# Kernel tuning notes

Hardware: AMD Instinct MI355X
Metric: run time of the kernel (lower is better)

The kernel has to match this reference:

```python
import jax, jax.numpy as jnp
import numpy as np

DT = 0.02
TMAX = 3.0
NUM_T = 151  # arange(0, Tmax+dt, dt) -> indices 0..150, 150*dt == Tmax == nonspike
THRESH = 1.0
TIMELINE = jnp.arange(NUM_T, dtype=jnp.float32) * DT          # [T]
TIMELINE_REV = jnp.flip(TIMELINE) + 0.1                        # [T]


def linear_spike_fwd(ti, W):
    """ti: [B, Fin] spike times; W: [Fout, Fin] -> out: [B, Fout] spike times."""
    # ramp: relu(t - ti)  -> [B, Fin, T]
    tmp = jax.nn.relu(TIMELINE[None, None, :] - ti[:, :, None])
    # membrane voltage: mem[b,j,t] = sum_i W[j,i] * tmp[b,i,t]  -> [B, Fout, T]
    mem = jnp.einsum('bit,ji->bjt', tmp, W)
    binary = (mem >= THRESH).astype(jnp.float32)
    binary = binary.at[:, :, -1].set(1.0)  # force spike at last timestep
    # reversed-timeline weighting makes argmax pick the FIRST spike index
    idx = jnp.argmax(binary * TIMELINE_REV, axis=2)
    return idx.astype(jnp.float32) * DT


def setup_inputs() -> dict:
    key = jax.random.key(0)
    k1, k2, k3 = jax.random.split(key, 3)
    B, F0, F1, F2 = 64, 1876, 1024, 10
    ti = jax.random.uniform(k1, (B, F0), dtype=jnp.float32)  # spike times in [0,1)
    W1 = 0.002 + 0.002 * jax.random.normal(k2, (F1, F0), dtype=jnp.float32)
    W2 = 0.001 + 0.001 * jax.random.normal(k3, (F2, F1), dtype=jnp.float32)
    return {"ti": ti, "W1": W1, "W2": W2}


def reference(ti, W1, W2):
    h1 = linear_spike_fwd(ti, W1)
    h2 = linear_spike_fwd(h1, W2)
    return h2
```

## Files before the change

### kernel.cpp

```cpp
#include <hip/hip_runtime.h>
#include <stdint.h>

namespace {

constexpr int   B_    = 64;
constexpr int   F0_   = 1876;
constexpr int   F1_   = 1024;
constexpr int   F2_   = 10;
constexpr int   NT_   = 151;
constexpr float DT_   = 0.02f;
constexpr int   NSTR_ = 2048;
constexpr int   CHUNK_= 256;
constexpr int   NGRP_ = 32;
constexpr int   NB1_  = 51;
constexpr float SCL_  = 67108864.0f;
constexpr float ISCL_ = 1.0f / 67108864.0f;

constexpr size_t OFF_W1T  = 0;
constexpr size_t OFF_PAIR = 7688192;
constexpr size_t OFF_IDX1 = OFF_PAIR + 1048576;

__global__ __launch_bounds__(256) void k_w1t(const float* __restrict__ W1,
                                             float* __restrict__ W1T) {
  __shared__ float tile[64][65];
  const int i0 = blockIdx.x * 64;
  const int j0 = blockIdx.y * 64;
  const int t  = threadIdx.x;
  const int c  = t & 63, r4 = t >> 6;
  for (int jj = r4; jj < 64; jj += 4) {
    int i = i0 + c;
    float v = (i < F0_) ? W1[(size_t)(j0 + jj) * F0_ + i] : 0.0f;
    tile[c][jj] = v;
  }
  __syncthreads();
  for (int ii = r4; ii < 64; ii += 4) {
    int i = i0 + ii;
    if (i <= F0_) W1T[(size_t)i * F1_ + j0 + c] = tile[ii][c];
  }
}

__global__ __launch_bounds__(256) void k_sort1(const float* __restrict__ ti,
                                               uint2* __restrict__ sPair) {
  __shared__ uint32_t hist[256][NB1_];
  __shared__ uint32_t bstart[NB1_ + 1];
  const int b = blockIdx.x, t = threadIdx.x;
  for (int k = 0; k < NB1_; ++k) hist[t][k] = 0;
  __syncthreads();

  const float* tib = ti + (size_t)b * F0_;
  const int n0 = t * 8;
  const int n1 = (n0 + 8 < F0_) ? n0 + 8 : F0_;
  for (int n = n0; n < n1; ++n) {
    int k = (int)ceilf(tib[n] * 50.0f);
    k = k < 0 ? 0 : (k > 50 ? 50 : k);
    hist[t][k]++;
  }
  __syncthreads();

  if (t < NB1_) {
    uint32_t run = 0;
    for (int c = 0; c < 256; ++c) { uint32_t x = hist[c][t]; hist[c][t] = run; run += x; }
    bstart[t + 1] = run;
  }
  __syncthreads();
  if (t == 0) {
    bstart[0] = 0;
    uint32_t acc = 0;
    for (int k = 0; k < NB1_; ++k) { uint32_t c = bstart[k + 1]; bstart[k + 1] = acc + c; acc += c; }
  }
  __syncthreads();

  uint2* out = sPair + (size_t)b * NSTR_;
  for (int n = n0; n < n1; ++n) {
    float v = tib[n];
    int k = (int)ceilf(v * 50.0f);
    k = k < 0 ? 0 : (k > 50 ? 50 : k);
    uint32_t pos = bstart[k] + hist[t][k]++;
    out[pos] = make_uint2(((uint32_t)n << 12) | (uint32_t)k, __float_as_uint(v));
  }
  for (int s = t; s < NSTR_ - F0_; s += 256)
    out[F0_ + s] = make_uint2(((uint32_t)F0_ << 12) | 80u, __float_as_uint(1.6f));
}

__global__ __launch_bounds__(512) void k_main1(const uint2* __restrict__ sPair,
                                               const float* __restrict__ W1T,
                                               uint8_t* __restrict__ idx1) {
  __shared__ int binAi[NB1_][128];
  __shared__ int binCi[NB1_][128];
  __shared__ int cand[4][128];
  const int blk  = blockIdx.x;
  const int b    = blk >> 3;
  const int jp   = blk & 7;
  const int tid  = threadIdx.x;
  const int lane = tid & 63;
  const int wv   = __builtin_amdgcn_readfirstlane(tid >> 6);

  {
    int4* p = (int4*)(&binAi[0][0]);
    const int ntot = (NB1_ * 128 * 2) / 4;
    for (int s = tid; s < ntot; s += 512) p[s] = make_int4(0, 0, 0, 0);
  }
  __syncthreads();

  const uint2* __restrict__ spw = sPair + (size_t)b * NSTR_ + wv * CHUNK_;
  const char*  __restrict__ wb  = (const char*)W1T;
  const uint32_t col8 = (uint32_t)(jp * 512 + lane * 8);

  float SA0 = 0.f, SC0 = 0.f, SA1 = 0.f, SC1 = 0.f;
  float SA0p = 0.f, SC0p = 0.f, SA1p = 0.f, SC1p = 0.f;
  uint32_t kcur;

  uint2  Pb[4][8];
  float2 W[4][8];

#define RDP(buf, g) {                                                         \
  _Pragma("unroll") for (int e = 0; e < 8; ++e) Pb[buf][e] = spw[(g) * 8 + e]; }

#define ISSW(buf) {                                                           \
  _Pragma("unroll") for (int e = 0; e < 8; ++e) {                             \
    W[buf][e] = *(const float2*)(wb + (Pb[buf][e].x & ~4095u) + col8); } }

#define DUMP() { if (kcur < (uint32_t)NB1_) {                                 \
    atomicAdd(&binAi[kcur][2 * lane],     __float2int_rn((SA0 - SA0p) * SCL_)); \
    atomicAdd(&binCi[kcur][2 * lane],     __float2int_rn((SC0 - SC0p) * SCL_)); \
    atomicAdd(&binAi[kcur][2 * lane + 1], __float2int_rn((SA1 - SA1p) * SCL_)); \
    atomicAdd(&binCi[kcur][2 * lane + 1], __float2int_rn((SC1 - SC1p) * SCL_)); } \
  SA0p = SA0; SC0p = SC0; SA1p = SA1; SC1p = SC1; }

#define PROC(buf) {                                                           \
  uint32_t kend = Pb[buf][7].x & 4095u;                                       \
  if (kend == kcur) {            \
    _Pragma("unroll") for (int e = 0; e < 8; ++e) {                           \
      float2 w = W[buf][e];                                                   \
      float tiv = __uint_as_float(Pb[buf][e].y);                              \
      SA0 += w.x; SC0 = fmaf(w.x, tiv, SC0);                                  \
      SA1 += w.y; SC1 = fmaf(w.y, tiv, SC1); }                                \
  } else {                                                                    \
    _Pragma("unroll") for (int e = 0; e < 8; ++e) {                           \
      uint32_t kb = Pb[buf][e].x & 4095u;                                     \
      if (kb != kcur) { DUMP(); kcur = kb; }                                  \
      float2 w = W[buf][e];                                                   \
      float tiv = __uint_as_float(Pb[buf][e].y);                              \
      SA0 += w.x; SC0 = fmaf(w.x, tiv, SC0);                                  \
      SA1 += w.y; SC1 = fmaf(w.y, tiv, SC1); }                                \
  } }

#define HALF(b0, b1, b2, b3, g)                                               \
  ISSW(b2); PROC(b0); RDP(b0, (g) + 4);                                       \
  ISSW(b3); PROC(b1); RDP(b1, (g) + 5);

  RDP(0, 0); RDP(1, 1); RDP(2, 2); RDP(3, 3);
  ISSW(0); ISSW(1);
  kcur = Pb[0][0].x & 4095u;

#pragma unroll 1
  for (int g = 0; g <= NGRP_ - 8; g += 4) {
    HALF(0, 1, 2, 3, g);
    HALF(2, 3, 0, 1, g + 2);
  }
  ISSW(2); PROC(0);
  ISSW(3); PROC(1);
  PROC(2); PROC(3);
  DUMP();

#undef HALF
#undef PROC
#undef DUMP
#undef ISSW
#undef RDP

  __syncthreads();

  {
    const int jh = wv & 1, tq = wv >> 1;
    const int col = jh * 64 + lane;
    float SA2 = 0.f, SC2 = 0.f;
    int cnd = 151;
    const int t0 = tq * 38;
    const int t1 = (tq == 3) ? NT_ : t0 + 38;
    for (int t = 0; t < t1; ++t) {
      if (t < NB1_) {
        SA2 += (float)binAi[t][col] * ISCL_;
        SC2 += (float)binCi[t][col] * ISCL_;
      }
      if (t >= t0 && cnd == 151) {
        float m = (float)t * DT_ * SA2 - SC2;
        if (m >= 1.0f) cnd = t;
      }
    }
    cand[tq][col] = cnd;
  }
  __syncthreads();
  if (tid < 128) {
    int id = min(min(cand[0][tid], cand[1][tid]),
                 min(cand[2][tid], cand[3][tid]));
    id = min(id, NT_ - 1);
    idx1[((size_t)b << 10) + (jp << 7) + tid] = (uint8_t)id;
  }
}

__global__ __launch_bounds__(256) void k_main2(const uint8_t* __restrict__ idx1,
                                               const float* __restrict__ W2,
                                               float* __restrict__ out) {
  __shared__ float wrow[F1_];
  __shared__ float tirow[F1_];
  __shared__ float part[4][3][64];
  const int blk = blockIdx.x;
  const int b   = blk / 10;
  const int j   = blk - b * 10;
  const int tid = threadIdx.x;
  const int lane = tid & 63, wvv = tid >> 6;

  const float*   w = W2  + (size_t)j * F1_;
  const uint8_t* h = idx1 + (size_t)b * F1_;
  for (int s = tid; s < F1_; s += 256) {
    wrow[s]  = w[s];
    tirow[s] = (float)h[s] * DT_;
  }
  __syncthreads();

  const float tl0 = (float)lane * DT_;
  const float tl1 = (float)(lane + 64) * DT_;
  const float tl2 = (float)(lane + 128) * DT_;
  float m0 = 0.f, m1 = 0.f, m2 = 0.f;
  const int i0 = wvv * 256;
#pragma unroll 4
  for (int i = i0; i < i0 + 256; ++i) {
    float tiv = tirow[i], ww = wrow[i];
    m0 = fmaf(ww, fmaxf(tl0 - tiv, 0.f), m0);
    m1 = fmaf(ww, fmaxf(tl1 - tiv, 0.f), m1);
    m2 = fmaf(ww, fmaxf(tl2 - tiv, 0.f), m2);
  }
  part[wvv][0][lane] = m0;
  part[wvv][1][lane] = m1;
  part[wvv][2][lane] = m2;
  __syncthreads();

  if (wvv == 0) {
    m0 = part[0][0][lane] + part[1][0][lane] + part[2][0][lane] + part[3][0][lane];
    m1 = part[0][1][lane] + part[1][1][lane] + part[2][1][lane] + part[3][1][lane];
    m2 = part[0][2][lane] + part[1][2][lane] + part[2][2][lane] + part[3][2][lane];
    unsigned long long b0 = __ballot(m0 >= 1.0f);
    unsigned long long b1 = __ballot(m1 >= 1.0f);
    unsigned long long b2 = __ballot(m2 >= 1.0f);
    b2 &= (1ull << 23) - 1;
    b2 |= (1ull << 22);
    int tres;
    if (b0)      tres = __ffsll((long long)b0) - 1;
    else if (b1) tres = 64 + __ffsll((long long)b1) - 1;
    else         tres = 128 + __ffsll((long long)b2) - 1;
    if (lane == 0) out[(size_t)b * F2_ + j] = (float)tres * DT_;
  }
}

}

extern "C" void kernel_launch(void* const* d_in, const int* in_sizes, int n_in,
                              void* d_out, int out_size, void* d_ws, size_t ws_size,
                              hipStream_t stream) {
  const float* ti = (const float*)d_in[0];
  const float* W1 = (const float*)d_in[1];
  const float* W2 = (const float*)d_in[2];
  float* out = (float*)d_out;

  char* ws = (char*)d_ws;
  float*   W1T  = (float*)(ws + OFF_W1T);
  uint2*   sPr  = (uint2*)(ws + OFF_PAIR);
  uint8_t* idx1 = (uint8_t*)(ws + OFF_IDX1);

  hipLaunchKernelGGL(k_w1t,   dim3(30, 16), dim3(256), 0, stream, W1, W1T);
  hipLaunchKernelGGL(k_sort1, dim3(64),     dim3(256), 0, stream, ti, sPr);
  hipLaunchKernelGGL(k_main1, dim3(512),    dim3(512), 0, stream, sPr, W1T, idx1);
  hipLaunchKernelGGL(k_main2, dim3(640),    dim3(256), 0, stream, idx1, W2, out);
}
```

Before: 80.05 us.

## Fuse transpose and sort kernels, pad bins to groups, stage pairs in LDS

Merges the W1 transpose and the per-batch bucket sort into one prep launch, which removes a kernel launch. Each time bin is padded to a multiple of 8 entries, and a per-group bin id is written so the main loop checks for a bin change once per group using a uniform scalar. The sorted pairs and group bins are copied into shared memory before the main loop, and the loop becomes a 3-stage rotation over 42 groups per wave. Columns of W1T are permuted so the per-lane atomics hit contiguous addresses. The trade-off is extra padding work (2688 entries instead of 2048) and more LDS per block, which may reduce occupancy.

Result: slower. 84.23 us (+5.2%).

```diff
diff --git a/kernel.cpp b/kernel.cpp
--- a/kernel.cpp
+++ b/kernel.cpp
@@ -9,82 +9,107 @@
 constexpr int   F2_   = 10;
 constexpr int   NT_   = 151;
 constexpr float DT_   = 0.02f;
-constexpr int   NSTR_ = 2048;
-constexpr int   CHUNK_= 256;
-constexpr int   NGRP_ = 32;
 constexpr int   NB1_  = 51;
+constexpr int   NSTR_ = 2688;
+constexpr int   NGT_  = 336;
+constexpr int   GPW_  = 42;
+constexpr int   ROWB_ = 4096;
 constexpr float SCL_  = 67108864.0f;
 constexpr float ISCL_ = 1.0f / 67108864.0f;
 
 constexpr size_t OFF_W1T  = 0;
 constexpr size_t OFF_PAIR = 7688192;
-constexpr size_t OFF_IDX1 = OFF_PAIR + 1048576;
-
-__global__ __launch_bounds__(256) void k_w1t(const float* __restrict__ W1,
-                                             float* __restrict__ W1T) {
-  __shared__ float tile[64][65];
-  const int i0 = blockIdx.x * 64;
-  const int j0 = blockIdx.y * 64;
-  const int t  = threadIdx.x;
-  const int c  = t & 63, r4 = t >> 6;
-  for (int jj = r4; jj < 64; jj += 4) {
-    int i = i0 + c;
-    float v = (i < F0_) ? W1[(size_t)(j0 + jj) * F0_ + i] : 0.0f;
-    tile[c][jj] = v;
-  }
-  __syncthreads();
-  for (int ii = r4; ii < 64; ii += 4) {
-    int i = i0 + ii;
-    if (i <= F0_) W1T[(size_t)i * F1_ + j0 + c] = tile[ii][c];
-  }
-}
-
-__global__ __launch_bounds__(256) void k_sort1(const float* __restrict__ ti,
-                                               uint2* __restrict__ sPair) {
-  __shared__ uint32_t hist[256][NB1_];
-  __shared__ uint32_t bstart[NB1_ + 1];
-  const int b = blockIdx.x, t = threadIdx.x;
-  for (int k = 0; k < NB1_; ++k) hist[t][k] = 0;
-  __syncthreads();
-
-  const float* tib = ti + (size_t)b * F0_;
-  const int n0 = t * 8;
-  const int n1 = (n0 + 8 < F0_) ? n0 + 8 : F0_;
-  for (int n = n0; n < n1; ++n) {
-    int k = (int)ceilf(tib[n] * 50.0f);
-    k = k < 0 ? 0 : (k > 50 ? 50 : k);
-    hist[t][k]++;
-  }
-  __syncthreads();
-
-  if (t < NB1_) {
-    uint32_t run = 0;
-    for (int c = 0; c < 256; ++c) { uint32_t x = hist[c][t]; hist[c][t] = run; run += x; }
-    bstart[t + 1] = run;
-  }
-  __syncthreads();
-  if (t == 0) {
-    bstart[0] = 0;
-    uint32_t acc = 0;
-    for (int k = 0; k < NB1_; ++k) { uint32_t c = bstart[k + 1]; bstart[k + 1] = acc + c; acc += c; }
-  }
-  __syncthreads();
-
-  uint2* out = sPair + (size_t)b * NSTR_;
-  for (int n = n0; n < n1; ++n) {
-    float v = tib[n];
-    int k = (int)ceilf(v * 50.0f);
-    k = k < 0 ? 0 : (k > 50 ? 50 : k);
-    uint32_t pos = bstart[k] + hist[t][k]++;
-    out[pos] = make_uint2(((uint32_t)n << 12) | (uint32_t)k, __float_as_uint(v));
-  }
-  for (int s = t; s < NSTR_ - F0_; s += 256)
-    out[F0_ + s] = make_uint2(((uint32_t)F0_ << 12) | 80u, __float_as_uint(1.6f));
-}
-
-__global__ __launch_bounds__(512) void k_main1(const uint2* __restrict__ sPair,
-                                               const float* __restrict__ W1T,
-                                               uint8_t* __restrict__ idx1) {
+constexpr size_t OFF_GB   = OFF_PAIR + 1376256;
+constexpr size_t OFF_IDX1 = OFF_GB + 86016;
+
+__global__ __launch_bounds__(256) void k_prep(const float* __restrict__ W1,
+                                              const float* __restrict__ ti,
+                                              float* __restrict__ W1Tp,
+                                              uint2* __restrict__ sPair,
+                                              uint32_t* __restrict__ gB) {
+  __shared__ uint32_t smem[13184];
+  const int t = threadIdx.x;
+  if (blockIdx.x < 480) {
+    float (*tile)[65] = (float (*)[65])smem;
+    const int bx = blockIdx.x;
+    const int i0 = (bx % 30) * 64;
+    const int j0 = (bx / 30) * 64;
+    const int c = t & 63, r4 = t >> 6;
+    for (int jj = r4; jj < 64; jj += 4) {
+      int i = i0 + c;
+      tile[c][jj] = (i < F0_) ? W1[(size_t)(j0 + jj) * F0_ + i] : 0.0f;
+    }
+    __syncthreads();
+    for (int ii = r4; ii < 64; ii += 4) {
+      int i = i0 + ii;
+      if (i <= F0_) {
+        int j = j0 + c;
+        int jp = j >> 7, r = j & 127;
+        int pc = (jp << 7) + ((r & 63) << 1) + (r >> 6);
+        W1Tp[(size_t)i * F1_ + pc] = tile[ii][c];
+      }
+    }
+  } else {
+    uint32_t (*hist)[NB1_] = (uint32_t (*)[NB1_])smem;
+    uint32_t* pstart = smem + 256 * NB1_;
+    uint32_t* cnts   = pstart + 52;
+    const int b = blockIdx.x - 480;
+    for (int k = 0; k < NB1_; ++k) hist[t][k] = 0;
+    __syncthreads();
+
+    const float* tib = ti + (size_t)b * F0_;
+    const int n0 = t * 8, n1 = (n0 + 8 < F0_) ? n0 + 8 : F0_;
+    for (int n = n0; n < n1; ++n) {
+      int k = (int)ceilf(tib[n] * 50.0f);
+      k = k < 0 ? 0 : (k > 50 ? 50 : k);
+      hist[t][k]++;
+    }
+    __syncthreads();
+
+    if (t < NB1_) {
+      uint32_t run = 0;
+      for (int c = 0; c < 256; ++c) { uint32_t x = hist[c][t]; hist[c][t] = run; run += x; }
+      cnts[t] = run;
+    }
+    __syncthreads();
+    if (t == 0) {
+      uint32_t acc = 0;
+      pstart[0] = 0;
+      for (int k = 0; k < NB1_; ++k) {
+        acc += (cnts[k] + 7u) & ~7u;
+        pstart[k + 1] = acc;
+      }
+    }
+    __syncthreads();
+
+    const uint32_t PT = pstart[NB1_];
+    uint2*    out = sPair + (size_t)b * NSTR_;
+    uint32_t* gb  = gB + (size_t)b * NGT_;
+    const uint2 dummy = make_uint2((uint32_t)F0_ * (uint32_t)ROWB_, 0u);
+
+    for (int n = n0; n < n1; ++n) {
+      float v = tib[n];
+      int k = (int)ceilf(v * 50.0f);
+      k = k < 0 ? 0 : (k > 50 ? 50 : k);
+      uint32_t pos = pstart[k] + hist[t][k]++;
+      out[pos] = make_uint2((uint32_t)n * (uint32_t)ROWB_, __float_as_uint(v));
+    }
+    if (t < NB1_) {
+      uint32_t s0 = pstart[t] + cnts[t], s1 = pstart[t + 1];
+      for (uint32_t s = s0; s < s1; ++s) out[s] = dummy;
+      for (uint32_t g = pstart[t] >> 3; g < (s1 >> 3); ++g) gb[g] = (uint32_t)t;
+    }
+    for (uint32_t s = PT + t; s < (uint32_t)NSTR_; s += 256) out[s] = dummy;
+    for (uint32_t g = (PT >> 3) + t; g < (uint32_t)NGT_; g += 256) gb[g] = 80u;
+  }
+}
+
+__global__ __launch_bounds__(512, 4) void k_main1(const uint2* __restrict__ sPair,
+                                                  const uint32_t* __restrict__ gB,
+                                                  const float* __restrict__ W1Tp,
+                                                  uint8_t* __restrict__ idx1) {
+  __shared__ uint2    pr[NSTR_];
+  __shared__ uint32_t gbw[NGT_];
   __shared__ int binAi[NB1_][128];
   __shared__ int binCi[NB1_][128];
   __shared__ int cand[4][128];
@@ -96,78 +121,69 @@
   const int wv   = __builtin_amdgcn_readfirstlane(tid >> 6);
 
   {
+    const uint4* src = (const uint4*)(sPair + (size_t)b * NSTR_);
+    uint4* dst = (uint4*)pr;
+    for (int s = tid; s < NSTR_ / 2; s += 512) dst[s] = src[s];
+    const uint32_t* gsrc = gB + (size_t)b * NGT_;
+    for (int s = tid; s < NGT_; s += 512) gbw[s] = gsrc[s];
     int4* p = (int4*)(&binAi[0][0]);
-    const int ntot = (NB1_ * 128 * 2) / 4;
-    for (int s = tid; s < ntot; s += 512) p[s] = make_int4(0, 0, 0, 0);
-  }
-  __syncthreads();
-
-  const uint2* __restrict__ spw = sPair + (size_t)b * NSTR_ + wv * CHUNK_;
-  const char*  __restrict__ wb  = (const char*)W1T;
+    for (int s = tid; s < (NB1_ * 128 * 2) / 4; s += 512) p[s] = make_int4(0, 0, 0, 0);
+  }
+  __syncthreads();
+
+  const char* wb = (const char*)W1Tp;
   const uint32_t col8 = (uint32_t)(jp * 512 + lane * 8);
+  const int g0 = wv * GPW_;
 
   float SA0 = 0.f, SC0 = 0.f, SA1 = 0.f, SC1 = 0.f;
   float SA0p = 0.f, SC0p = 0.f, SA1p = 0.f, SC1p = 0.f;
   uint32_t kcur;
 
-  uint2  Pb[4][8];
-  float2 W[4][8];
-
-#define RDP(buf, g) {                                                         \
-  _Pragma("unroll") for (int e = 0; e < 8; ++e) Pb[buf][e] = spw[(g) * 8 + e]; }
-
-#define ISSW(buf) {                                                           \
+  uint32_t rA[8], rB[8], rC[8], hA, hB, hC;
+  float    tA[8], tB[8], tC[8];
+  float2   WA[8], WB[8], WC[8];
+
+#define LOADP(S, g) { const int gg = (g) <= (NGT_ - 1) ? (g) : (NGT_ - 1);    \
+  _Pragma("unroll") for (int q = 0; q < 4; ++q) {                             \
+    uint4 x = *(const uint4*)(&pr[gg * 8 + q * 2]);                           \
+    r##S[2 * q]     = x.x; t##S[2 * q]     = __uint_as_float(x.y);            \
+    r##S[2 * q + 1] = x.z; t##S[2 * q + 1] = __uint_as_float(x.w); }          \
+  h##S = gbw[gg]; }
+
+#define ISSW(S) { _Pragma("unroll") for (int e = 0; e < 8; ++e)               \
+    W##S[e] = *(const float2*)(wb + (size_t)(r##S[e] + col8)); }
+
+#define DUMP() { if (kcur < (uint32_t)NB1_) {                                 \
+    atomicAdd(&binAi[kcur][lane],      __float2int_rn((SA0 - SA0p) * SCL_));  \
+    atomicAdd(&binCi[kcur][lane],      __float2int_rn((SC0 - SC0p) * SCL_));  \
+    atomicAdd(&binAi[kcur][64 + lane], __float2int_rn((SA1 - SA1p) * SCL_));  \
+    atomicAdd(&binCi[kcur][64 + lane], __float2int_rn((SC1 - SC1p) * SCL_)); }\
+  SA0p = SA0; SC0p = SC0; SA1p = SA1; SC1p = SC1; }
+
+#define PROC(S) {                                                             \
+  uint32_t kg = __builtin_amdgcn_readfirstlane(h##S);                         \
+  if (kg != kcur) { DUMP(); kcur = kg; }                                      \
   _Pragma("unroll") for (int e = 0; e < 8; ++e) {                             \
-    W[buf][e] = *(const float2*)(wb + (Pb[buf][e].x & ~4095u) + col8); } }
-
-#define DUMP() { if (kcur < (uint32_t)NB1_) {                                 \
-    atomicAdd(&binAi[kcur][2 * lane],     __float2int_rn((SA0 - SA0p) * SCL_)); \
-    atomicAdd(&binCi[kcur][2 * lane],     __float2int_rn((SC0 - SC0p) * SCL_)); \
-    atomicAdd(&binAi[kcur][2 * lane + 1], __float2int_rn((SA1 - SA1p) * SCL_)); \
-    atomicAdd(&binCi[kcur][2 * lane + 1], __float2int_rn((SC1 - SC1p) * SCL_)); } \
-  SA0p = SA0; SC0p = SC0; SA1p = SA1; SC1p = SC1; }
-
-#define PROC(buf) {                                                           \
-  uint32_t kend = Pb[buf][7].x & 4095u;                                       \
-  if (kend == kcur) {            \
-    _Pragma("unroll") for (int e = 0; e < 8; ++e) {                           \
-      float2 w = W[buf][e];                                                   \
-      float tiv = __uint_as_float(Pb[buf][e].y);                              \
-      SA0 += w.x; SC0 = fmaf(w.x, tiv, SC0);                                  \
-      SA1 += w.y; SC1 = fmaf(w.y, tiv, SC1); }                                \
-  } else {                                                                    \
-    _Pragma("unroll") for (int e = 0; e < 8; ++e) {                           \
-      uint32_t kb = Pb[buf][e].x & 4095u;                                     \
-      if (kb != kcur) { DUMP(); kcur = kb; }                                  \
-      float2 w = W[buf][e];                                                   \
-      float tiv = __uint_as_float(Pb[buf][e].y);                              \
-      SA0 += w.x; SC0 = fmaf(w.x, tiv, SC0);                                  \
-      SA1 += w.y; SC1 = fmaf(w.y, tiv, SC1); }                                \
-  } }
-
-#define HALF(b0, b1, b2, b3, g)                                               \
-  ISSW(b2); PROC(b0); RDP(b0, (g) + 4);                                       \
-  ISSW(b3); PROC(b1); RDP(b1, (g) + 5);
-
-  RDP(0, 0); RDP(1, 1); RDP(2, 2); RDP(3, 3);
-  ISSW(0); ISSW(1);
-  kcur = Pb[0][0].x & 4095u;
+    SA0 += W##S[e].x; SC0 = fmaf(W##S[e].x, t##S[e], SC0);                    \
+    SA1 += W##S[e].y; SC1 = fmaf(W##S[e].y, t##S[e], SC1); } }
+
+  LOADP(A, g0); LOADP(B, g0 + 1);
+  ISSW(A); ISSW(B);
+  kcur = __builtin_amdgcn_readfirstlane(hA);
 
 #pragma unroll 1
-  for (int g = 0; g <= NGRP_ - 8; g += 4) {
-    HALF(0, 1, 2, 3, g);
-    HALF(2, 3, 0, 1, g + 2);
-  }
-  ISSW(2); PROC(0);
-  ISSW(3); PROC(1);
-  PROC(2); PROC(3);
+  for (int m = 0; m < GPW_ / 3; ++m) {
+    const int g = g0 + 3 * m;
+    LOADP(C, g + 2); PROC(A); ISSW(C);
+    LOADP(A, g + 3); PROC(B); ISSW(A);
+    LOADP(B, g + 4); PROC(C); ISSW(B);
+  }
   DUMP();
 
-#undef HALF
 #undef PROC
 #undef DUMP
 #undef ISSW
-#undef RDP
+#undef LOADP
 
   __syncthreads();
 
@@ -178,14 +194,14 @@
     int cnd = 151;
     const int t0 = tq * 38;
     const int t1 = (tq == 3) ? NT_ : t0 + 38;
-    for (int t = 0; t < t1; ++t) {
-      if (t < NB1_) {
-        SA2 += (float)binAi[t][col] * ISCL_;
-        SC2 += (float)binCi[t][col] * ISCL_;
-      }
-      if (t >= t0 && cnd == 151) {
-        float m = (float)t * DT_ * SA2 - SC2;
-        if (m >= 1.0f) cnd = t;
+    for (int tt = 0; tt < t1; ++tt) {
+      if (tt < NB1_) {
+        SA2 += (float)binAi[tt][col] * ISCL_;
+        SC2 += (float)binCi[tt][col] * ISCL_;
+      }
+      if (tt >= t0 && cnd == 151) {
+        float m = (float)tt * DT_ * SA2 - SC2;
+        if (m >= 1.0f) cnd = tt;
       }
     }
     cand[tq][col] = cnd;
@@ -264,12 +280,12 @@
   float* out = (float*)d_out;
 
   char* ws = (char*)d_ws;
-  float*   W1T  = (float*)(ws + OFF_W1T);
-  uint2*   sPr  = (uint2*)(ws + OFF_PAIR);
-  uint8_t* idx1 = (uint8_t*)(ws + OFF_IDX1);
-
-  hipLaunchKernelGGL(k_w1t,   dim3(30, 16), dim3(256), 0, stream, W1, W1T);
-  hipLaunchKernelGGL(k_sort1, dim3(64),     dim3(256), 0, stream, ti, sPr);
-  hipLaunchKernelGGL(k_main1, dim3(512),    dim3(512), 0, stream, sPr, W1T, idx1);
-  hipLaunchKernelGGL(k_main2, dim3(640),    dim3(256), 0, stream, idx1, W2, out);
-}
+  float*    W1Tp = (float*)(ws + OFF_W1T);
+  uint2*    sPr  = (uint2*)(ws + OFF_PAIR);
+  uint32_t* gBp  = (uint32_t*)(ws + OFF_GB);
+  uint8_t*  idx1 = (uint8_t*)(ws + OFF_IDX1);
+
+  hipLaunchKernelGGL(k_prep,  dim3(544), dim3(256), 0, stream, W1, ti, W1Tp, sPr, gBp);
+  hipLaunchKernelGGL(k_main1, dim3(512), dim3(512), 0, stream, sPr, gBp, W1Tp, idx1);
+  hipLaunchKernelGGL(k_main2, dim3(640), dim3(256), 0, stream, idx1, W2, out);
+}
```
